# Kernel tuning notes

Hardware: AMD Instinct MI355X
Metric: run time of the kernel (lower is better)

Reference implementation:

```python
import jax, jax.numpy as jnp
import numpy as np
from jax import lax

EPS = 1e-5
ITERS = 10
PPI = 4  # pixels_per_iter


def conv2d(x, w, pad=0, groups=1):
    return lax.conv_general_dilated(
        x, w, (1, 1), [(pad, pad), (pad, pad)],
        dimension_numbers=('NCHW', 'OIHW', 'NCHW'), feature_group_count=groups)


def sep_conv(x, dw, pw):
    # depthwise 3x3 (groups=C) then pointwise 1x1, bias-free
    return conv2d(conv2d(x, dw, pad=1, groups=x.shape[1]), pw)


def maxpool(x, k):
    return lax.reduce_window(x, -jnp.inf, lax.max, (1, 1, k, k), (1, 1, k, k), 'VALID')


def avgpool(x, k):
    return lax.reduce_window(x, 0., lax.add, (1, 1, k, k), (1, 1, k, k), 'VALID') / (k * k)


def grid_sample(img, grid):
    # torch.nn.functional.grid_sample, bilinear, align_corners=True, zeros padding
    # img [B,C,H,W], grid [B,H,W,2] with grid[...,0]=x(width), grid[...,1]=y(height)
    B, C, H, W = img.shape
    x = (grid[..., 0] + 1.) * 0.5 * (W - 1)
    y = (grid[..., 1] + 1.) * 0.5 * (H - 1)
    x0 = jnp.floor(x)
    y0 = jnp.floor(y)
    wx = x - x0
    wy = y - y0

    def corner(xf, yf, w):
        valid = (xf >= 0) & (xf <= W - 1) & (yf >= 0) & (yf <= H - 1)
        xi = jnp.clip(xf, 0, W - 1).astype(jnp.int32)
        yi = jnp.clip(yf, 0, H - 1).astype(jnp.int32)
        v = jax.vmap(lambda im, yy, xx: im[:, yy, xx])(img, yi, xi)  # [B,C,H,W]
        return v * (w * valid)[:, None, :, :]

    return (corner(x0, y0, (1 - wx) * (1 - wy)) + corner(x0 + 1, y0, wx * (1 - wy))
            + corner(x0, y0 + 1, (1 - wx) * wy) + corner(x0 + 1, y0 + 1, wx * wy))


def upmat(n_in, n_out):
    # bilinear interpolation matrix, align_corners=True (UpsamplingBilinear2d)
    pos = jnp.arange(n_out) * ((n_in - 1) / (n_out - 1))
    i0 = jnp.floor(pos).astype(jnp.int32)
    i1 = jnp.minimum(i0 + 1, n_in - 1)
    w = pos - i0
    r = jnp.arange(n_out)
    return jnp.zeros((n_out, n_in), jnp.float32).at[r, i0].add(1 - w).at[r, i1].add(w)


def setup_inputs() -> dict:
    key = jax.random.key(0)
    ks = jax.random.split(key, 12)
    B, Cin, Cout, H, W = 4, 256, 256, 128, 128
    s = 0.05
    d = {}
    d['x'] = jax.random.normal(ks[0], (B, Cin, H, W), jnp.float32)
    d['grads'] = jax.random.normal(ks[1], (B, 2, H, W), jnp.float32)
    d['bn_gamma'] = jnp.ones((Cin,), jnp.float32)
    d['bn_beta'] = jnp.zeros((Cin,), jnp.float32)
    d['bn_mean'] = jnp.zeros((Cin,), jnp.float32)
    d['bn_var'] = jnp.ones((Cin,), jnp.float32)
    d['att1_dw'] = jax.random.normal(ks[2], (Cin, 1, 3, 3), jnp.float32) * s
    d['att1_pw'] = jax.random.normal(ks[3], (Cout, Cin, 1, 1), jnp.float32) * s
    d['att2_dw'] = jax.random.normal(ks[4], (Cin, 1, 3, 3), jnp.float32) * s
    d['att2_pw'] = jax.random.normal(ks[5], (Cout, Cin, 1, 1), jnp.float32) * s
    d['conv1_w'] = jax.random.normal(ks[6], (Cout, Cin, 1, 1), jnp.float32) * s
    d['conv2_w'] = jax.random.normal(ks[7], (Cout, Cin, 1, 1), jnp.float32) * s
    d['add1_w'] = jax.random.normal(ks[8], (Cout, 2 * Cout, 1, 1), jnp.float32) * s
    d['add2_w'] = jax.random.normal(ks[9], (Cout, 2 * Cout, 1, 1), jnp.float32) * s
    d['merge_dw'] = jax.random.normal(ks[10], (2 * Cout, 1, 3, 3), jnp.float32) * s
    d['merge_pw'] = jax.random.normal(ks[11], (Cout, 2 * Cout, 1, 1), jnp.float32) * s
    return d


def reference(x, grads, bn_gamma, bn_beta, bn_mean, bn_var,
              att1_dw, att1_pw, att2_dw, att2_pw, conv1_w, conv2_w,
              add1_w, add2_w, merge_dw, merge_pw):
    # BatchNorm (eval mode, running stats)
    scale = (bn_gamma / jnp.sqrt(bn_var + EPS))[None, :, None, None]
    x = (x - bn_mean[None, :, None, None]) * scale + bn_beta[None, :, None, None]

    a1 = jax.nn.sigmoid(sep_conv(x, att1_dw, att1_pw))
    a2 = jax.nn.sigmoid(sep_conv(x, att2_dw, att2_pw))
    m1 = conv2d(x, conv1_w)
    m2 = conv2d(x, conv2_w)

    a1 = maxpool(a1, PPI)
    a2 = maxpool(a2, PPI)
    m1 = maxpool(m1, PPI)
    m2 = maxpool(m2, PPI)

    B, _, Hd, Wd = m1.shape
    g = avgpool(grads, PPI) / Hd           # [B,2,Hd,Wd]
    g = jnp.transpose(g, (0, 2, 3, 1))      # [B,Hd,Wd,2]

    # identity affine_grid, align_corners=True
    gx = jnp.broadcast_to(jnp.linspace(-1., 1., Wd)[None, None, :], (B, Hd, Wd))
    gy = jnp.broadcast_to(jnp.linspace(-1., 1., Hd)[None, :, None], (B, Hd, Wd))
    base = jnp.stack([gx, gy], axis=-1)
    grid1 = base + g
    grid2 = base - g

    m1 = jax.nn.relu(m1)
    m2 = jax.nn.relu(m2)
    m1_sum, m2_sum = m1, m2
    for _ in range(ITERS):
        m1 = grid_sample(m1, grid1) * a1
        m2 = grid_sample(m2, grid2) * a2
        m1_sum = conv2d(jnp.concatenate([m1_sum, m1], axis=1), add1_w)
        m2_sum = conv2d(jnp.concatenate([m2_sum, m2], axis=1), add2_w)

    out = sep_conv(jnp.concatenate([m1_sum, m2_sum], axis=1) / ITERS, merge_dw, merge_pw)

    Mh = upmat(Hd, Hd * PPI)
    Mw = upmat(Wd, Wd * PPI)
    return jnp.einsum('oh,bchw,pw->bcop', Mh, out, Mw)
```

## Files before the change

kernel.cpp:

```cpp
#include <hip/hip_runtime.h>
#include <cstddef>
#include <cstdint>

#define BN_EPS 1e-5f
typedef unsigned short ushort_t;
typedef __attribute__((ext_vector_type(8))) short bf16x8;
typedef __attribute__((ext_vector_type(4))) float f32x4;

__device__ __forceinline__ ushort_t f2bf(float f) {
  unsigned u = __float_as_uint(f);
  unsigned r = (u + 0x7fffu + ((u >> 16) & 1u)) >> 16;
  return (ushort_t)r;
}
__device__ __forceinline__ float bf2f(ushort_t h) {
  return __uint_as_float(((unsigned)h) << 16);
}
__device__ __forceinline__ void unp8(uint4 u, ushort_t* d) {
  d[0] = u.x & 0xffff; d[1] = u.x >> 16;
  d[2] = u.y & 0xffff; d[3] = u.y >> 16;
  d[4] = u.z & 0xffff; d[5] = u.z >> 16;
  d[6] = u.w & 0xffff; d[7] = u.w >> 16;
}
__device__ __forceinline__ uint4 pk8(const ushort_t* d) {
  uint4 u;
  u.x = (unsigned)d[0] | ((unsigned)d[1] << 16);
  u.y = (unsigned)d[2] | ((unsigned)d[3] << 16);
  u.z = (unsigned)d[4] | ((unsigned)d[5] << 16);
  u.w = (unsigned)d[6] | ((unsigned)d[7] << 16);
  return u;
}

__global__ __launch_bounds__(256) void wsplit_kernel(
    const float* s0, const float* s1, const float* s2, const float* s3,
    const float* s4, const float* s5, const float* s6, ushort_t* d0,
    ushort_t* d1, ushort_t* d2, ushort_t* d3, ushort_t* d4, ushort_t* d5,
    ushort_t* d6) {
  int r = blockIdx.x;
  int tid = threadIdx.x;
  if (r < 1024) {
    int wi = r >> 8, oc = r & 255;
    const float* s = wi == 0 ? s0 : wi == 1 ? s1 : wi == 2 ? s2 : s3;
    ushort_t* d = wi == 0 ? d0 : wi == 1 ? d1 : wi == 2 ? d2 : d3;
    float v = s[oc * 256 + tid];
    ushort_t h = f2bf(v);
// ... 37 lines not shown
    if (rr < 0 || rr > 127) continue;
    const float* rp = base + rr * 128;
    float4 v = reinterpret_cast<const float4*>(rp)[col4];
    v.x = fmaf(v.x, s, sh);
    v.y = fmaf(v.y, s, sh);
    v.z = fmaf(v.z, s, sh);
    v.w = fmaf(v.w, s, sh);
    float lf = col4 ? fmaf(rp[col4 * 4 - 1], s, sh) : 0.f;
    float rg = (col4 < 31) ? fmaf(rp[col4 * 4 + 4], s, sh) : 0.f;
    float k0 = w[(dr + 1) * 3 + 0];
    float k1 = w[(dr + 1) * 3 + 1];
    float k2 = w[(dr + 1) * 3 + 2];
    acc.x = fmaf(k0, lf, fmaf(k1, v.x, fmaf(k2, v.y, acc.x)));
    acc.y = fmaf(k0, v.x, fmaf(k1, v.y, fmaf(k2, v.z, acc.y)));
    acc.z = fmaf(k0, v.y, fmaf(k1, v.z, fmaf(k2, v.w, acc.z)));
    acc.w = fmaf(k0, v.z, fmaf(k1, v.w, fmaf(k2, rg, acc.w)));
  }
  reinterpret_cast<float4*>(out + (size_t)bc * 16384 + row * 128)[col4] = acc;
}

__global__ __launch_bounds__(256) void pw_mfma_kernel(
    const float* __restrict__ src0, const float* __restrict__ src1,
    const ushort_t* __restrict__ W0, const ushort_t* __restrict__ W1,
    ushort_t* __restrict__ o0h, ushort_t* __restrict__ o0l,
    ushort_t* __restrict__ o1h, ushort_t* __restrict__ o1l,
    const float* __restrict__ gamma, const float* __restrict__ beta,
    const float* __restrict__ mean, const float* __restrict__ var, int bnflag,
    int act) {
  __shared__ ushort_t Xh[64 * 40], Xl[64 * 40];
  __shared__ ushort_t Wh[256 * 40], Wl[256 * 40];
  __shared__ float s_lds[256], sh_lds[256];
  const int tid = threadIdx.x;
  const int bx = blockIdx.x;
  const int pr = bx >> 3, pcs = bx & 7;
  const int b = blockIdx.y, z = blockIdx.z;
  const float* src = z ? src1 : src0;
  const ushort_t* Wq = z ? W1 : W0;
  ushort_t* ohi = z ? o1h : o0h;
  ushort_t* olo = z ? o1l : o0l;
  const int R0 = pr * 4, C0 = pcs * 16;
  if (bnflag) {
    float sv = gamma[tid] * rsqrtf(var[tid] + BN_EPS);
    s_lds[tid] = sv;
    sh_lds[tid] = beta[tid] - mean[tid] * sv;
  }
  const int w = tid >> 6, l = tid & 63, lr = l & 15, lh = l >> 4;
  f32x4 acc[4][4];
#pragma unroll
  for (int i = 0; i < 4; i++)
#pragma unroll
    for (int j = 0; j < 4; j++) acc[i][j] = 0.f;

  for (int kc = 0; kc < 8; ++kc) {
    int ic0 = kc * 32;
    __syncthreads();
#pragma unroll
    for (int p = 0; p < 2; ++p) {
      int idx = p * 256 + tid;
      int ic = idx >> 4, rc = idx & 15, r = rc >> 2, c4 = rc & 3;
      const float* gp =
          src + (((size_t)(b * 256 + ic0 + ic) * 128 + R0 + r) * 128 + C0 +
                 c4 * 4);
      float4 v = *(const float4*)gp;
      if (bnflag) {
        float s = s_lds[ic0 + ic], sh = sh_lds[ic0 + ic];
        v.x = fmaf(v.x, s, sh);
        v.y = fmaf(v.y, s, sh);
        v.z = fmaf(v.z, s, sh);
        v.w = fmaf(v.w, s, sh);
      }
      int baserow = c4 * 16 + r * 4;
      const float* vp = &v.x;
#pragma unroll
      for (int q = 0; q < 4; ++q) {
        float f = vp[q];
        ushort_t hv = f2bf(f);
        Xh[(baserow + q) * 40 + ic] = hv;
        Xl[(baserow + q) * 40 + ic] = f2bf(f - bf2f(hv));
      }
    }
#pragma unroll
    for (int p = 0; p < 4; ++p) {
      int i = p * 256 + tid;
      int oc = i >> 2, slot = i & 3;
      *(uint4*)(&Wh[oc * 40 + slot * 8]) =
          *(const uint4*)(Wq + (size_t)oc * 512 + ic0 + slot * 8);
      *(uint4*)(&Wl[oc * 40 + slot * 8]) =
          *(const uint4*)(Wq + (size_t)oc * 512 + 256 + ic0 + slot * 8);
    }
    __syncthreads();
    bf16x8 ah[4], al[4], bh[4], bl[4];
#pragma unroll
    for (int mt = 0; mt < 4; ++mt) {
      ah[mt] = *(const bf16x8*)(&Xh[(mt * 16 + lr) * 40 + lh * 8]);
      al[mt] = *(const bf16x8*)(&Xl[(mt * 16 + lr) * 40 + lh * 8]);
    }
#pragma unroll
    for (int nt = 0; nt < 4; ++nt) {
      bh[nt] = *(const bf16x8*)(&Wh[(w * 64 + nt * 16 + lr) * 40 + lh * 8]);
      bl[nt] = *(const bf16x8*)(&Wl[(w * 64 + nt * 16 + lr) * 40 + lh * 8]);
    }
#pragma unroll
    for (int mt = 0; mt < 4; ++mt)
#pragma unroll
      for (int nt = 0; nt < 4; ++nt)
        acc[mt][nt] = __builtin_amdgcn_mfma_f32_16x16x32_bf16(
            ah[mt], bh[nt], acc[mt][nt], 0, 0, 0);
#pragma unroll
    for (int mt = 0; mt < 4; ++mt)
#pragma unroll
      for (int nt = 0; nt < 4; ++nt)
        acc[mt][nt] = __builtin_amdgcn_mfma_f32_16x16x32_bf16(
            al[mt], bh[nt], acc[mt][nt], 0, 0, 0);
#pragma unroll
    for (int mt = 0; mt < 4; ++mt)
#pragma unroll
      for (int nt = 0; nt < 4; ++nt)
        acc[mt][nt] = __builtin_amdgcn_mfma_f32_16x16x32_bf16(
            ah[mt], bl[nt], acc[mt][nt], 0, 0, 0);
  }
#pragma unroll
  for (int mt = 0; mt < 4; ++mt) {
    int ppx = pr * 32 + pcs * 4 + mt;
#pragma unroll
    for (int nt = 0; nt < 4; ++nt) {
      f32x4 v = acc[mt][nt];
      float m0 = fmaxf(fmaxf(v[0], v[1]), fmaxf(v[2], v[3]));
      m0 = fmaxf(m0, __shfl_xor(m0, 16));
      m0 = fmaxf(m0, __shfl_xor(m0, 32));
      float r = act ? fmaxf(m0, 0.f) : 1.f / (1.f + expf(-m0));
      ushort_t hv = f2bf(r);
      ushort_t lv = f2bf(r - bf2f(hv));
      if (l < 16) {
        size_t o = (size_t)(b * 1024 + ppx) * 256 + w * 64 + nt * 16 + lr;
        ohi[o] = hv;
        olo[o] = lv;
      }
    }
  }
}

__global__ __launch_bounds__(256) void cat_mfma_kernel(
    const ushort_t* Ah0, const ushort_t* Al0, const ushort_t* Bh0,
    const ushort_t* Bl0, const ushort_t* Wq0, ushort_t* oh0, ushort_t* ol0,
    float* of0, const ushort_t* Ah1, const ushort_t* Al1, const ushort_t* Bh1,
    const ushort_t* Bl1, const ushort_t* Wq1, ushort_t* oh1, ushort_t* ol1,
    float* of1, int CA, int sA, int sB, int fout) {
  __shared__ ushort_t Xh[64 * 40], Xl[64 * 40];
  __shared__ ushort_t Wh[128 * 40], Wl[128 * 40];
  __shared__ unsigned obuf[64 * 132];
  const int tid = threadIdx.x;
  const int PX0 = blockIdx.x * 64;
  const int b = blockIdx.y >> 1, OC0 = (blockIdx.y & 1) * 128;
  const int z = blockIdx.z;
  const ushort_t* Ah = z ? Ah1 : Ah0;
  const ushort_t* Al = z ? Al1 : Al0;
  const ushort_t* Bh = z ? Bh1 : Bh0;
  const ushort_t* Bl = z ? Bl1 : Bl0;
  const ushort_t* Wq = z ? Wq1 : Wq0;
  ushort_t* ohi = z ? oh1 : oh0;
  ushort_t* olo = z ? ol1 : ol0;
  float* of = z ? of1 : of0;
  const int w = tid >> 6, l = tid & 63, lr = l & 15, lh = l >> 4;
  f32x4 acc[4][2];
#pragma unroll
  for (int i = 0; i < 4; i++)
#pragma unroll
    for (int j = 0; j < 2; j++) acc[i][j] = 0.f;

  for (int kc = 0; kc < 16; ++kc) {
    int k0 = kc * 32;
    __syncthreads();
    {
      const ushort_t *xh, *xl;
      int cc0, st;
      if (k0 < CA) {
        xh = Ah; xl = Al; cc0 = k0; st = sA;
      } else {
        xh = Bh; xl = Bl; cc0 = k0 - CA; st = sB;
      }
      int px = tid >> 2, slot = tid & 3;
      size_t xo = (size_t)(b * 1024 + PX0 + px) * st + cc0 + slot * 8;
      *(uint4*)(&Xh[px * 40 + slot * 8]) = *(const uint4*)(xh + xo);
      *(uint4*)(&Xl[px * 40 + slot * 8]) = *(const uint4*)(xl + xo);
    }
#pragma unroll
    for (int p = 0; p < 2; ++p) {
      int i = p * 256 + tid;
      int oc = i >> 2, slot = i & 3;
      *(uint4*)(&Wh[oc * 40 + slot * 8]) =
          *(const uint4*)(Wq + (size_t)(OC0 + oc) * 1024 + k0 + slot * 8);
      *(uint4*)(&Wl[oc * 40 + slot * 8]) = *(const uint4*)(
          Wq + (size_t)(OC0 + oc) * 1024 + 512 + k0 + slot * 8);
    }
    __syncthreads();
    bf16x8 ah[4], al[4], bh[2], bl[2];
#pragma unroll
    for (int mt = 0; mt < 4; ++mt) {
      ah[mt] = *(const bf16x8*)(&Xh[(mt * 16 + lr) * 40 + lh * 8]);
      al[mt] = *(const bf16x8*)(&Xl[(mt * 16 + lr) * 40 + lh * 8]);
    }
#pragma unroll
    for (int nt = 0; nt < 2; ++nt) {
      bh[nt] = *(const bf16x8*)(&Wh[(w * 32 + nt * 16 + lr) * 40 + lh * 8]);
      bl[nt] = *(const bf16x8*)(&Wl[(w * 32 + nt * 16 + lr) * 40 + lh * 8]);
    }
#pragma unroll
    for (int mt = 0; mt < 4; ++mt)
#pragma unroll
      for (int nt = 0; nt < 2; ++nt)
        acc[mt][nt] = __builtin_amdgcn_mfma_f32_16x16x32_bf16(
            ah[mt], bh[nt], acc[mt][nt], 0, 0, 0);
#pragma unroll
    for (int mt = 0; mt < 4; ++mt)
#pragma unroll
      for (int nt = 0; nt < 2; ++nt)
        acc[mt][nt] = __builtin_amdgcn_mfma_f32_16x16x32_bf16(
            al[mt], bh[nt], acc[mt][nt], 0, 0, 0);
#pragma unroll
    for (int mt = 0; mt < 4; ++mt)
#pragma unroll
      for (int nt = 0; nt < 2; ++nt)
        acc[mt][nt] = __builtin_amdgcn_mfma_f32_16x16x32_bf16(
            ah[mt], bl[nt], acc[mt][nt], 0, 0, 0);
  }
  if (fout) {
#pragma unroll
    for (int mt = 0; mt < 4; ++mt)
#pragma unroll
      for (int nt = 0; nt < 2; ++nt) {
        int oc = OC0 + w * 32 + nt * 16 + lr;
        int px0 = PX0 + mt * 16 + lh * 4;
        float4 vv = make_float4(acc[mt][nt][0], acc[mt][nt][1], acc[mt][nt][2],
                                acc[mt][nt][3]);
        *(float4*)(of + ((size_t)(b * 256 + oc) * 1024 + px0)) = vv;
      }
  } else {
    __syncthreads();
#pragma unroll
    for (int mt = 0; mt < 4; ++mt)
#pragma unroll
      for (int nt = 0; nt < 2; ++nt)
#pragma unroll
        for (int j = 0; j < 4; ++j) {
          float f = acc[mt][nt][j];
          ushort_t hv = f2bf(f);
          ushort_t lv = f2bf(f - bf2f(hv));
          obuf[(mt * 16 + lh * 4 + j) * 132 + w * 32 + nt * 16 + lr] =
              (unsigned)hv | ((unsigned)lv << 16);
        }
    __syncthreads();
    int px = tid >> 2;
#pragma unroll
    for (int g = 0; g < 4; ++g) {
      int og = (tid & 3) * 32 + g * 8;
      ushort_t h8[8], l8[8];
#pragma unroll
      for (int q = 0; q < 8; ++q) {
        unsigned u = obuf[px * 132 + og + q];
        h8[q] = u & 0xffff;
        l8[q] = u >> 16;
      }
      size_t o = (size_t)(b * 1024 + PX0 + px) * 256 + OC0 + og;
      *(uint4*)(ohi + o) = pk8(h8);
      *(uint4*)(olo + o) = pk8(l8);
    }
  }
}

__global__ void grads_pool_kernel(const float* __restrict__ grads,
                                  int4* __restrict__ pxi1,
                                  float4* __restrict__ w1,
                                  int4* __restrict__ pxi2,
                                  float4* __restrict__ w2) {
  unsigned flat = blockIdx.x * 256u + threadIdx.x;
  unsigned pw = flat & 31u, ph = (flat >> 5) & 31u, b = flat >> 10;
  const float* gx = grads + (size_t)(b * 2 + 0) * 16384;
  const float* gy = grads + (size_t)(b * 2 + 1) * 16384;
  float sx_ = 0.f, sy_ = 0.f;
#pragma unroll
  for (int r = 0; r < 4; r++) {
    const float* rx = gx + (ph * 4 + r) * 128 + pw * 4;
    const float* ry = gy + (ph * 4 + r) * 128 + pw * 4;
#pragma unroll
    for (int q = 0; q < 4; q++) {
      sx_ += rx[q];
      sy_ += ry[q];
    }
  }
// ... 14 lines not shown
    bool vx1 = (x0f + 1.f >= 0.f) && (x0f + 1.f <= 31.f);
    bool vy0 = (y0f >= 0.f) && (y0f <= 31.f);
    bool vy1 = (y0f + 1.f >= 0.f) && (y0f + 1.f <= 31.f);
    int x0c = min(max(x0, 0), 31), x1c = min(max(x0 + 1, 0), 31);
    int y0c = min(max(y0, 0), 31), y1c = min(max(y0 + 1, 0), 31);
    int4 pi = make_int4(y0c * 32 + x0c, y0c * 32 + x1c, y1c * 32 + x0c,
                        y1c * 32 + x1c);
    float4 ww =
        make_float4((1.f - wx) * (1.f - wy) * ((vx0 && vy0) ? 1.f : 0.f),
                    wx * (1.f - wy) * ((vx1 && vy0) ? 1.f : 0.f),
                    (1.f - wx) * wy * ((vx0 && vy1) ? 1.f : 0.f),
                    wx * wy * ((vx1 && vy1) ? 1.f : 0.f));
    if (s == 0) {
      pxi1[sidx] = pi;
      w1[sidx] = ww;
    } else {
      pxi2[sidx] = pi;
      w2[sidx] = ww;
    }
  }
}

__global__ __launch_bounds__(256) void gs_mul_kernel(
    const ushort_t* c0h, const ushort_t* c0l, const ushort_t* a0h,
    const ushort_t* a0l, const int4* pxi0, const float4* wg0, ushort_t* o0h,
    ushort_t* o0l, const ushort_t* c1h, const ushort_t* c1l,
    const ushort_t* a1h, const ushort_t* a1l, const int4* pxi1,
    const float4* wg1, ushort_t* o1h, ushort_t* o1l) {
  unsigned flat = blockIdx.x * 256u + threadIdx.x;
  unsigned cg = flat & 31u;
  unsigned px = (flat >> 5) & 1023u;
  unsigned b = (flat >> 15) & 3u;
  unsigned br = flat >> 17;
  const ushort_t* ch = br ? c1h : c0h;
  const ushort_t* cl = br ? c1l : c0l;
  const ushort_t* ah = br ? a1h : a0h;
  const ushort_t* al = br ? a1l : a0l;
  const int4* pxi = br ? pxi1 : pxi0;
  const float4* wg = br ? wg1 : wg0;
  ushort_t* ohp = br ? o1h : o0h;
  ushort_t* olp = br ? o1l : o0l;
  int4 pi = pxi[b * 1024 + px];
  float4 wv = wg[b * 1024 + px];
  size_t rb = (size_t)b * 1024;
  int co = cg * 8;
  float v[8];
#pragma unroll
  for (int j = 0; j < 8; ++j) v[j] = 0.f;
  const int rows[4] = {pi.x, pi.y, pi.z, pi.w};
  const float wks[4] = {wv.x, wv.y, wv.z, wv.w};
#pragma unroll
  for (int k = 0; k < 4; ++k) {
    size_t o = (rb + rows[k]) * 256 + co;
    uint4 hu = *(const uint4*)(ch + o);
    uint4 lu = *(const uint4*)(cl + o);
    ushort_t h8[8], l8[8];
    unp8(hu, h8);
    unp8(lu, l8);
    float wk = wks[k];
#pragma unroll
    for (int j = 0; j < 8; ++j)
      v[j] = fmaf(wk, bf2f(h8[j]) + bf2f(l8[j]), v[j]);
  }
  size_t oo = (rb + px) * 256 + co;
  uint4 ahu = *(const uint4*)(ah + oo);
  uint4 alu = *(const uint4*)(al + oo);
  ushort_t ah8[8], al8[8];
  unp8(ahu, ah8);
  unp8(alu, al8);
  ushort_t rh[8], rl[8];
#pragma unroll
  for (int j = 0; j < 8; ++j) {
    float r = v[j] * (bf2f(ah8[j]) + bf2f(al8[j]));
    rh[j] = f2bf(r);
    rl[j] = f2bf(r - bf2f(rh[j]));
  }
  *(uint4*)(ohp + oo) = pk8(rh);
  *(uint4*)(olp + oo) = pk8(rl);
}

__global__ __launch_bounds__(256) void merge_dw_kernel(
    const ushort_t* s1h, const ushort_t* s1l, const ushort_t* s2h,
    const ushort_t* s2l, const float* __restrict__ wall, ushort_t* dh,
    ushort_t* dl) {
  __shared__ float wlds[576];
  int bx = blockIdx.x;
  int pr = bx >> 3, cset = bx & 7;
  int b = blockIdx.y;
  int pc = threadIdx.x & 31, cg = threadIdx.x >> 5;
  for (int i = threadIdx.x; i < 576; i += 256) wlds[i] = wall[cset * 576 + i];
  __syncthreads();
  const ushort_t* sh_ = (cset < 4) ? s1h : s2h;
  const ushort_t* sl_ = (cset < 4) ? s1l : s2l;
  int csrc = (cset & 3) * 64 + cg * 8;
  float acc[8];
#pragma unroll
  for (int j = 0; j < 8; ++j) acc[j] = 0.f;
#pragma unroll
  for (int dr = -1; dr <= 1; ++dr) {
    int r2 = pr + dr;
    if (r2 < 0 || r2 > 31) continue;
#pragma unroll
    for (int dc = -1; dc <= 1; ++dc) {
      int c2 = pc + dc;
      if (c2 < 0 || c2 > 31) continue;
      size_t o = ((size_t)(b * 1024) + r2 * 32 + c2) * 256 + csrc;
      uint4 hu = *(const uint4*)(sh_ + o);
      uint4 lu = *(const uint4*)(sl_ + o);
      ushort_t h8[8], l8[8];
      unp8(hu, h8);
      unp8(lu, l8);
      int wi = (dr + 1) * 3 + (dc + 1);
#pragma unroll
      for (int j = 0; j < 8; ++j)
        acc[j] = fmaf(wlds[(cg * 8 + j) * 9 + wi], bf2f(h8[j]) + bf2f(l8[j]),
                      acc[j]);
    }
  }
  size_t oo = ((size_t)(b * 1024) + pr * 32 + pc) * 512 + cset * 64 + cg * 8;
  ushort_t h8[8], l8[8];
#pragma unroll
  for (int j = 0; j < 8; ++j) {
    float f = acc[j] * 0.1f;
    h8[j] = f2bf(f);
    l8[j] = f2bf(f - bf2f(h8[j]));
  }
  *(uint4*)(dh + oo) = pk8(h8);
  *(uint4*)(dl + oo) = pk8(l8);
}

__global__ __launch_bounds__(256) void upsample_kernel(
    const float* __restrict__ mid, float* __restrict__ out) {
  unsigned flat = blockIdx.x * 256u + threadIdx.x;
  unsigned ow4 = flat & 31u;
  unsigned oh = (flat >> 5) & 127u;
  unsigned bc = flat >> 12;
  const float* pl = mid + (size_t)bc * 1024;
  float rh = oh * (31.f / 127.f);
  float ihf = floorf(rh);
  float wh = rh - ihf;
  int i0 = (int)ihf;
  int i1 = min(i0 + 1, 31);
  const float* r0 = pl + i0 * 32;
  const float* r1 = pl + i1 * 32;
  float4 res;
  float* rp = &res.x;
#pragma unroll
  for (int j = 0; j < 4; j++) {
    unsigned ow = ow4 * 4 + j;
    float rw = ow * (31.f / 127.f);
    float jwf = floorf(rw);
// ... 23 lines not shown
  const float* att1_dw = (const float*)d_in[6];
  const float* att1_pw = (const float*)d_in[7];
  const float* att2_dw = (const float*)d_in[8];
  const float* att2_pw = (const float*)d_in[9];
  const float* conv1_w = (const float*)d_in[10];
  const float* conv2_w = (const float*)d_in[11];
  const float* add1_w = (const float*)d_in[12];
  const float* add2_w = (const float*)d_in[13];
  const float* merge_dww = (const float*)d_in[14];
  const float* merge_pww = (const float*)d_in[15];
  float* out = (float*)d_out;

  const size_t MB = 1u << 20;
  uint8_t* base = (uint8_t*)d_ws;
  float* t1 = (float*)base;
  uint8_t* P = base + 64 * MB;
  ushort_t* wAtt1 = (ushort_t*)P; P += 262144;
  ushort_t* wAtt2 = (ushort_t*)P; P += 262144;
  ushort_t* wC1 = (ushort_t*)P; P += 262144;
  ushort_t* wC2 = (ushort_t*)P; P += 262144;
  ushort_t* wAdd1 = (ushort_t*)P; P += 524288;
  ushort_t* wAdd2 = (ushort_t*)P; P += 524288;
  ushort_t* wMrg = (ushort_t*)P; P += 524288;
  ushort_t* a1h = (ushort_t*)P; P += 2 * MB;
  ushort_t* a1l = (ushort_t*)P; P += 2 * MB;
  ushort_t* a2h = (ushort_t*)P; P += 2 * MB;
  ushort_t* a2l = (ushort_t*)P; P += 2 * MB;
  ushort_t* m1Ph = (ushort_t*)P; P += 2 * MB;
  ushort_t* m1Pl = (ushort_t*)P; P += 2 * MB;
  ushort_t* m2Ph = (ushort_t*)P; P += 2 * MB;
  ushort_t* m2Pl = (ushort_t*)P; P += 2 * MB;
  int4* pxi1 = (int4*)P; P += 65536;
  float4* w1g = (float4*)P; P += 65536;
  int4* pxi2 = (int4*)P; P += 65536;
  float4* w2g = (float4*)P; P += 65536;
  uint8_t* Q = base;
  ushort_t* m1Qh = (ushort_t*)Q; Q += 2 * MB;
  ushort_t* m1Ql = (ushort_t*)Q; Q += 2 * MB;
  ushort_t* m2Qh = (ushort_t*)Q; Q += 2 * MB;
  ushort_t* m2Ql = (ushort_t*)Q; Q += 2 * MB;
  ushort_t* s1ah = (ushort_t*)Q; Q += 2 * MB;
  ushort_t* s1al = (ushort_t*)Q; Q += 2 * MB;
  ushort_t* s1bh = (ushort_t*)Q; Q += 2 * MB;
  ushort_t* s1bl = (ushort_t*)Q; Q += 2 * MB;
  ushort_t* s2ah = (ushort_t*)Q; Q += 2 * MB;
  ushort_t* s2al = (ushort_t*)Q; Q += 2 * MB;
  ushort_t* s2bh = (ushort_t*)Q; Q += 2 * MB;
  ushort_t* s2bl = (ushort_t*)Q; Q += 2 * MB;
  ushort_t* dwmh = (ushort_t*)Q; Q += 4 * MB;
  ushort_t* dwml = (ushort_t*)Q; Q += 4 * MB;
  float* mid = (float*)Q; Q += 4 * MB;

  wsplit_kernel<<<1792, 256, 0, stream>>>(att1_pw, att2_pw, conv1_w, conv2_w,
                                          add1_w, add2_w, merge_pww, wAtt1,
                                          wAtt2, wC1, wC2, wAdd1, wAdd2, wMrg);
  pw_mfma_kernel<<<dim3(256, 4, 2), 256, 0, stream>>>(
      x, x, wC1, wC2, m1Ph, m1Pl, m2Ph, m2Pl, bn_gamma, bn_beta, bn_mean,
      bn_var, 1, 1);
  dw_bn_kernel<<<16384, 256, 0, stream>>>(x, att1_dw, bn_gamma, bn_beta,
                                          bn_mean, bn_var, t1);
  pw_mfma_kernel<<<dim3(256, 4, 1), 256, 0, stream>>>(
      t1, t1, wAtt1, wAtt1, a1h, a1l, a1h, a1l, bn_gamma, bn_beta, bn_mean,
      bn_var, 0, 0);
  dw_bn_kernel<<<16384, 256, 0, stream>>>(x, att2_dw, bn_gamma, bn_beta,
                                          bn_mean, bn_var, t1);
  pw_mfma_kernel<<<dim3(256, 4, 1), 256, 0, stream>>>(
      t1, t1, wAtt2, wAtt2, a2h, a2l, a2h, a2l, bn_gamma, bn_beta, bn_mean,
      bn_var, 0, 0);
  grads_pool_kernel<<<16, 256, 0, stream>>>(grads, pxi1, w1g, pxi2, w2g);

  const ushort_t *c1h = m1Ph, *c1l = m1Pl, *c2h = m2Ph, *c2l = m2Pl;
  const ushort_t *ss1h = m1Ph, *ss1l = m1Pl, *ss2h = m2Ph, *ss2l = m2Pl;
  for (int it = 0; it < 10; ++it) {
    ushort_t* n1h = (it & 1) ? m1Ph : m1Qh;
    ushort_t* n1l = (it & 1) ? m1Pl : m1Ql;
    ushort_t* n2h = (it & 1) ? m2Ph : m2Qh;
    ushort_t* n2l = (it & 1) ? m2Pl : m2Ql;
    gs_mul_kernel<<<1024, 256, 0, stream>>>(c1h, c1l, a1h, a1l, pxi1, w1g, n1h,
                                            n1l, c2h, c2l, a2h, a2l, pxi2, w2g,
                                            n2h, n2l);
    ushort_t* so1h = (it & 1) ? s1bh : s1ah;
    ushort_t* so1l = (it & 1) ? s1bl : s1al;
    ushort_t* so2h = (it & 1) ? s2bh : s2ah;
    ushort_t* so2l = (it & 1) ? s2bl : s2al;
    cat_mfma_kernel<<<dim3(16, 8, 2), 256, 0, stream>>>(
        ss1h, ss1l, n1h, n1l, wAdd1, so1h, so1l, nullptr, ss2h, ss2l, n2h, n2l,
        wAdd2, so2h, so2l, nullptr, 256, 256, 256, 0);
    c1h = n1h; c1l = n1l; c2h = n2h; c2l = n2l;
    ss1h = so1h; ss1l = so1l; ss2h = so2h; ss2l = so2l;
  }
  merge_dw_kernel<<<dim3(256, 4), 256, 0, stream>>>(ss1h, ss1l, ss2h, ss2l,
                                                    merge_dww, dwmh, dwml);
  cat_mfma_kernel<<<dim3(16, 8, 1), 256, 0, stream>>>(
      dwmh, dwml, dwmh, dwml, wMrg, nullptr, nullptr, mid, dwmh, dwml, dwmh,
      dwml, wMrg, nullptr, nullptr, mid, 512, 512, 512, 1);
  upsample_kernel<<<16384, 256, 0, stream>>>(mid, out);
}
```

Measured before the change: 704.3 us.

## Interleave bf16 hi/lo pairs, prefetch GEMM tiles, shrink cat kernel tiles

Split-bf16 activations now use one interleaved 32-bit hi/lo word per value instead of two separate planes. Every producer and consumer (gs_mul, merge_dw, pointwise and cat GEMMs) switches to single vector loads and stores of the packed pairs. The pw and cat MFMA kernels register-prefetch the next K chunk while computing the current one. The cat kernel is replaced by a 128-thread, 32x64-tile version with direct global stores instead of the LDS-staged output transpose. This aims to cut memory transactions and hide load latency, but the direct scattered 4-byte output stores may be less coalesced.

After: 663.9 us. 5.7% less time.

```diff
diff --git a/kernel.cpp b/kernel.cpp
--- a/kernel.cpp
+++ b/kernel.cpp
@@ -15,11 +15,12 @@
 __device__ __forceinline__ float bf2f(ushort_t h) {
   return __uint_as_float(((unsigned)h) << 16);
 }
-__device__ __forceinline__ void unp8(uint4 u, ushort_t* d) {
-  d[0] = u.x & 0xffff; d[1] = u.x >> 16;
-  d[2] = u.y & 0xffff; d[3] = u.y >> 16;
-  d[4] = u.z & 0xffff; d[5] = u.z >> 16;
-  d[6] = u.w & 0xffff; d[7] = u.w >> 16;
+__device__ __forceinline__ float upk(unsigned u) {
+  return bf2f((ushort_t)(u & 0xffff)) + bf2f((ushort_t)(u >> 16));
+}
+__device__ __forceinline__ unsigned pkpair(float f) {
+  ushort_t h = f2bf(f);
+  return (unsigned)h | ((unsigned)f2bf(f - bf2f(h)) << 16);
 }
 __device__ __forceinline__ uint4 pk8(const ushort_t* d) {
   uint4 u;
@@ -103,8 +104,7 @@
 __global__ __launch_bounds__(256) void pw_mfma_kernel(
     const float* __restrict__ src0, const float* __restrict__ src1,
     const ushort_t* __restrict__ W0, const ushort_t* __restrict__ W1,
-    ushort_t* __restrict__ o0h, ushort_t* __restrict__ o0l,
-    ushort_t* __restrict__ o1h, ushort_t* __restrict__ o1l,
+    unsigned* __restrict__ o0, unsigned* __restrict__ o1,
     const float* __restrict__ gamma, const float* __restrict__ beta,
     const float* __restrict__ mean, const float* __restrict__ var, int bnflag,
     int act) {
@@ -117,14 +117,17 @@
   const int b = blockIdx.y, z = blockIdx.z;
   const float* src = z ? src1 : src0;
   const ushort_t* Wq = z ? W1 : W0;
-  ushort_t* ohi = z ? o1h : o0h;
-  ushort_t* olo = z ? o1l : o0l;
+  unsigned* op = z ? o1 : o0;
   const int R0 = pr * 4, C0 = pcs * 16;
   if (bnflag) {
     float sv = gamma[tid] * rsqrtf(var[tid] + BN_EPS);
     s_lds[tid] = sv;
     sh_lds[tid] = beta[tid] - mean[tid] * sv;
-  }
+  } else {
+    s_lds[tid] = 1.f;
+    sh_lds[tid] = 0.f;
+  }
+  __syncthreads();
   const int w = tid >> 6, l = tid & 63, lr = l & 15, lh = l >> 4;
   f32x4 acc[4][4];
 #pragma unroll
@@ -132,24 +135,34 @@
 #pragma unroll
     for (int j = 0; j < 4; j++) acc[i][j] = 0.f;
 
-  for (int kc = 0; kc < 8; ++kc) {
+  float4 xf0, xf1;
+  auto LDXP = [&](int kc) {
     int ic0 = kc * 32;
-    __syncthreads();
+    {
+      int idx = tid;
+      int ic = idx >> 4, rc = idx & 15, r = rc >> 2, c4 = rc & 3;
+      xf0 = *(const float4*)(src + (((size_t)(b * 256 + ic0 + ic) * 128 + R0 +
+                                     r) * 128 + C0 + c4 * 4));
+    }
+    {
+      int idx = 256 + tid;
+      int ic = idx >> 4, rc = idx & 15, r = rc >> 2, c4 = rc & 3;
+      xf1 = *(const float4*)(src + (((size_t)(b * 256 + ic0 + ic) * 128 + R0 +
+                                     r) * 128 + C0 + c4 * 4));
+    }
+  };
+  auto WRXP = [&](int kc) {
+    int ic0 = kc * 32;
 #pragma unroll
     for (int p = 0; p < 2; ++p) {
       int idx = p * 256 + tid;
       int ic = idx >> 4, rc = idx & 15, r = rc >> 2, c4 = rc & 3;
-      const float* gp =
-          src + (((size_t)(b * 256 + ic0 + ic) * 128 + R0 + r) * 128 + C0 +
-                 c4 * 4);
-      float4 v = *(const float4*)gp;
-      if (bnflag) {
-        float s = s_lds[ic0 + ic], sh = sh_lds[ic0 + ic];
-        v.x = fmaf(v.x, s, sh);
-        v.y = fmaf(v.y, s, sh);
-        v.z = fmaf(v.z, s, sh);
-        v.w = fmaf(v.w, s, sh);
-      }
+      float4 v = p ? xf1 : xf0;
+      float s = s_lds[ic0 + ic], sh = sh_lds[ic0 + ic];
+      v.x = fmaf(v.x, s, sh);
+      v.y = fmaf(v.y, s, sh);
+      v.z = fmaf(v.z, s, sh);
+      v.w = fmaf(v.w, s, sh);
       int baserow = c4 * 16 + r * 4;
       const float* vp = &v.x;
 #pragma unroll
@@ -160,6 +173,9 @@
         Xl[(baserow + q) * 40 + ic] = f2bf(f - bf2f(hv));
       }
     }
+  };
+  auto WSTG = [&](int kc) {
+    int ic0 = kc * 32;
 #pragma unroll
     for (int p = 0; p < 4; ++p) {
       int i = p * 256 + tid;
@@ -169,7 +185,13 @@
       *(uint4*)(&Wl[oc * 40 + slot * 8]) =
           *(const uint4*)(Wq + (size_t)oc * 512 + 256 + ic0 + slot * 8);
     }
-    __syncthreads();
+  };
+  LDXP(0);
+  WRXP(0);
+  WSTG(0);
+  __syncthreads();
+  for (int kc = 0; kc < 8; ++kc) {
+    if (kc < 7) LDXP(kc + 1);
     bf16x8 ah[4], al[4], bh[4], bl[4];
 #pragma unroll
     for (int mt = 0; mt < 4; ++mt) {
@@ -199,6 +221,12 @@
       for (int nt = 0; nt < 4; ++nt)
         acc[mt][nt] = __builtin_amdgcn_mfma_f32_16x16x32_bf16(
             ah[mt], bl[nt], acc[mt][nt], 0, 0, 0);
+    if (kc < 7) {
+      __syncthreads();
+      WRXP(kc + 1);
+      WSTG(kc + 1);
+      __syncthreads();
+    }
   }
 #pragma unroll
   for (int mt = 0; mt < 4; ++mt) {
@@ -210,74 +238,83 @@
       m0 = fmaxf(m0, __shfl_xor(m0, 16));
       m0 = fmaxf(m0, __shfl_xor(m0, 32));
       float r = act ? fmaxf(m0, 0.f) : 1.f / (1.f + expf(-m0));
-      ushort_t hv = f2bf(r);
-      ushort_t lv = f2bf(r - bf2f(hv));
-      if (l < 16) {
-        size_t o = (size_t)(b * 1024 + ppx) * 256 + w * 64 + nt * 16 + lr;
-        ohi[o] = hv;
-        olo[o] = lv;
-      }
-    }
-  }
-}
-
-__global__ __launch_bounds__(256) void cat_mfma_kernel(
-    const ushort_t* Ah0, const ushort_t* Al0, const ushort_t* Bh0,
-    const ushort_t* Bl0, const ushort_t* Wq0, ushort_t* oh0, ushort_t* ol0,
-    float* of0, const ushort_t* Ah1, const ushort_t* Al1, const ushort_t* Bh1,
-    const ushort_t* Bl1, const ushort_t* Wq1, ushort_t* oh1, ushort_t* ol1,
-    float* of1, int CA, int sA, int sB, int fout) {
-  __shared__ ushort_t Xh[64 * 40], Xl[64 * 40];
-  __shared__ ushort_t Wh[128 * 40], Wl[128 * 40];
-  __shared__ unsigned obuf[64 * 132];
+      if (l < 16)
+        op[(size_t)(b * 1024 + ppx) * 256 + w * 64 + nt * 16 + lr] = pkpair(r);
+    }
+  }
+}
+
+__global__ __launch_bounds__(128) void catp_kernel(
+    const unsigned* A0, const unsigned* B0, const ushort_t* W0, unsigned* op0,
+    float* of0, const unsigned* A1, const unsigned* B1, const ushort_t* W1,
+    unsigned* op1, float* of1, int CA, int sA, int sB, int fout) {
+  __shared__ ushort_t Xh[32 * 40], Xl[32 * 40];
+  __shared__ ushort_t Wh[64 * 40], Wl[64 * 40];
   const int tid = threadIdx.x;
-  const int PX0 = blockIdx.x * 64;
-  const int b = blockIdx.y >> 1, OC0 = (blockIdx.y & 1) * 128;
+  const int strip = blockIdx.x;
+  const int b = strip >> 5;
+  const int PX0 = (strip & 31) * 32;
+  const int OC0 = blockIdx.y * 64;
   const int z = blockIdx.z;
-  const ushort_t* Ah = z ? Ah1 : Ah0;
-  const ushort_t* Al = z ? Al1 : Al0;
-  const ushort_t* Bh = z ? Bh1 : Bh0;
-  const ushort_t* Bl = z ? Bl1 : Bl0;
-  const ushort_t* Wq = z ? Wq1 : Wq0;
-  ushort_t* ohi = z ? oh1 : oh0;
-  ushort_t* olo = z ? ol1 : ol0;
+  const unsigned* A = z ? A1 : A0;
+  const unsigned* B = z ? B1 : B0;
+  const ushort_t* Wq = z ? W1 : W0;
+  unsigned* op = z ? op1 : op0;
   float* of = z ? of1 : of0;
   const int w = tid >> 6, l = tid & 63, lr = l & 15, lh = l >> 4;
-  f32x4 acc[4][2];
-#pragma unroll
-  for (int i = 0; i < 4; i++)
+  const int spx = tid >> 2, sslot = tid & 3;
+  const int soc = tid >> 1, shalf = tid & 1;
+  uint4 xr0, xr1, w0h, w1h, w0l, w1l;
+  f32x4 acc[2][2];
+#pragma unroll
+  for (int i = 0; i < 2; i++)
 #pragma unroll
     for (int j = 0; j < 2; j++) acc[i][j] = 0.f;
 
+  auto LDX = [&](int kc) {
+    int k0 = kc * 32;
+    const unsigned* src;
+    int cc0, st;
+    if (k0 < CA) {
+      src = A; cc0 = k0; st = sA;
+    } else {
+      src = B; cc0 = k0 - CA; st = sB;
+    }
+    const unsigned* p =
+        src + ((size_t)(b * 1024 + PX0 + spx) * st + cc0 + sslot * 8);
+    xr0 = *(const uint4*)p;
+    xr1 = *(const uint4*)(p + 4);
+    const ushort_t* wp = Wq + (size_t)(OC0 + soc) * 1024 + k0 + shalf * 16;
+    w0h = *(const uint4*)wp;
+    w1h = *(const uint4*)(wp + 8);
+    w0l = *(const uint4*)(wp + 512);
+    w1l = *(const uint4*)(wp + 520);
+  };
+  auto WRX = [&]() {
+    ushort_t h8[8], l8[8];
+    h8[0] = xr0.x & 0xffff; l8[0] = xr0.x >> 16;
+    h8[1] = xr0.y & 0xffff; l8[1] = xr0.y >> 16;
+    h8[2] = xr0.z & 0xffff; l8[2] = xr0.z >> 16;
+    h8[3] = xr0.w & 0xffff; l8[3] = xr0.w >> 16;
+    h8[4] = xr1.x & 0xffff; l8[4] = xr1.x >> 16;
+    h8[5] = xr1.y & 0xffff; l8[5] = xr1.y >> 16;
+    h8[6] = xr1.z & 0xffff; l8[6] = xr1.z >> 16;
+    h8[7] = xr1.w & 0xffff; l8[7] = xr1.w >> 16;
+    *(uint4*)(&Xh[spx * 40 + sslot * 8]) = pk8(h8);
+    *(uint4*)(&Xl[spx * 40 + sslot * 8]) = pk8(l8);
+    *(uint4*)(&Wh[soc * 40 + shalf * 16]) = w0h;
+    *(uint4*)(&Wh[soc * 40 + shalf * 16 + 8]) = w1h;
+    *(uint4*)(&Wl[soc * 40 + shalf * 16]) = w0l;
+    *(uint4*)(&Wl[soc * 40 + shalf * 16 + 8]) = w1l;
+  };
+  LDX(0);
+  WRX();
+  __syncthreads();
   for (int kc = 0; kc < 16; ++kc) {
-    int k0 = kc * 32;
-    __syncthreads();
-    {
-      const ushort_t *xh, *xl;
-      int cc0, st;
-      if (k0 < CA) {
-        xh = Ah; xl = Al; cc0 = k0; st = sA;
-      } else {
-        xh = Bh; xl = Bl; cc0 = k0 - CA; st = sB;
-      }
-      int px = tid >> 2, slot = tid & 3;
-      size_t xo = (size_t)(b * 1024 + PX0 + px) * st + cc0 + slot * 8;
-      *(uint4*)(&Xh[px * 40 + slot * 8]) = *(const uint4*)(xh + xo);
-      *(uint4*)(&Xl[px * 40 + slot * 8]) = *(const uint4*)(xl + xo);
-    }
-#pragma unroll
-    for (int p = 0; p < 2; ++p) {
-      int i = p * 256 + tid;
-      int oc = i >> 2, slot = i & 3;
-      *(uint4*)(&Wh[oc * 40 + slot * 8]) =
-          *(const uint4*)(Wq + (size_t)(OC0 + oc) * 1024 + k0 + slot * 8);
-      *(uint4*)(&Wl[oc * 40 + slot * 8]) = *(const uint4*)(
-          Wq + (size_t)(OC0 + oc) * 1024 + 512 + k0 + slot * 8);
-    }
-    __syncthreads();
-    bf16x8 ah[4], al[4], bh[2], bl[2];
-#pragma unroll
-    for (int mt = 0; mt < 4; ++mt) {
+    if (kc < 15) LDX(kc + 1);
+    bf16x8 ah[2], al[2], bh[2], bl[2];
+#pragma unroll
+    for (int mt = 0; mt < 2; ++mt) {
       ah[mt] = *(const bf16x8*)(&Xh[(mt * 16 + lr) * 40 + lh * 8]);
       al[mt] = *(const bf16x8*)(&Xl[(mt * 16 + lr) * 40 + lh * 8]);
     }
@@ -287,27 +324,25 @@
       bl[nt] = *(const bf16x8*)(&Wl[(w * 32 + nt * 16 + lr) * 40 + lh * 8]);
     }
 #pragma unroll
-    for (int mt = 0; mt < 4; ++mt)
-#pragma unroll
-      for (int nt = 0; nt < 2; ++nt)
+    for (int mt = 0; mt < 2; ++mt)
+#pragma unroll
+      for (int nt = 0; nt < 2; ++nt) {
         acc[mt][nt] = __builtin_amdgcn_mfma_f32_16x16x32_bf16(
             ah[mt], bh[nt], acc[mt][nt], 0, 0, 0);
-#pragma unroll
-    for (int mt = 0; mt < 4; ++mt)
-#pragma unroll
-      for (int nt = 0; nt < 2; ++nt)
         acc[mt][nt] = __builtin_amdgcn_mfma_f32_16x16x32_bf16(
             al[mt], bh[nt], acc[mt][nt], 0, 0, 0);
-#pragma unroll
-    for (int mt = 0; mt < 4; ++mt)
-#pragma unroll
-      for (int nt = 0; nt < 2; ++nt)
         acc[mt][nt] = __builtin_amdgcn_mfma_f32_16x16x32_bf16(
             ah[mt], bl[nt], acc[mt][nt], 0, 0, 0);
+      }
+    if (kc < 15) {
+      __syncthreads();
+      WRX();
+      __syncthreads();
+    }
   }
   if (fout) {
 #pragma unroll
-    for (int mt = 0; mt < 4; ++mt)
+    for (int mt = 0; mt < 2; ++mt)
 #pragma unroll
       for (int nt = 0; nt < 2; ++nt) {
         int oc = OC0 + w * 32 + nt * 16 + lr;
@@ -317,35 +352,17 @@
         *(float4*)(of + ((size_t)(b * 256 + oc) * 1024 + px0)) = vv;
       }
   } else {
-    __syncthreads();
-#pragma unroll
-    for (int mt = 0; mt < 4; ++mt)
-#pragma unroll
-      for (int nt = 0; nt < 2; ++nt)
+#pragma unroll
+    for (int mt = 0; mt < 2; ++mt)
+#pragma unroll
+      for (int nt = 0; nt < 2; ++nt) {
+        int oc = OC0 + w * 32 + nt * 16 + lr;
 #pragma unroll
         for (int j = 0; j < 4; ++j) {
-          float f = acc[mt][nt][j];
-          ushort_t hv = f2bf(f);
-          ushort_t lv = f2bf(f - bf2f(hv));
-          obuf[(mt * 16 + lh * 4 + j) * 132 + w * 32 + nt * 16 + lr] =
-              (unsigned)hv | ((unsigned)lv << 16);
+          int px = PX0 + mt * 16 + lh * 4 + j;
+          op[(size_t)(b * 1024 + px) * 256 + oc] = pkpair(acc[mt][nt][j]);
         }
-    __syncthreads();
-    int px = tid >> 2;
-#pragma unroll
-    for (int g = 0; g < 4; ++g) {
-      int og = (tid & 3) * 32 + g * 8;
-      ushort_t h8[8], l8[8];
-#pragma unroll
-      for (int q = 0; q < 8; ++q) {
-        unsigned u = obuf[px * 132 + og + q];
-        h8[q] = u & 0xffff;
-        l8[q] = u >> 16;
       }
-      size_t o = (size_t)(b * 1024 + PX0 + px) * 256 + OC0 + og;
-      *(uint4*)(ohi + o) = pk8(h8);
-      *(uint4*)(olo + o) = pk8(l8);
-    }
   }
 }
 
@@ -406,24 +423,19 @@
 }
 
 __global__ __launch_bounds__(256) void gs_mul_kernel(
-    const ushort_t* c0h, const ushort_t* c0l, const ushort_t* a0h,
-    const ushort_t* a0l, const int4* pxi0, const float4* wg0, ushort_t* o0h,
-    ushort_t* o0l, const ushort_t* c1h, const ushort_t* c1l,
-    const ushort_t* a1h, const ushort_t* a1l, const int4* pxi1,
-    const float4* wg1, ushort_t* o1h, ushort_t* o1l) {
+    const unsigned* c0, const unsigned* a0, const int4* pxi0,
+    const float4* wg0, unsigned* o0, const unsigned* c1, const unsigned* a1,
+    const int4* pxi1, const float4* wg1, unsigned* o1) {
   unsigned flat = blockIdx.x * 256u + threadIdx.x;
   unsigned cg = flat & 31u;
   unsigned px = (flat >> 5) & 1023u;
   unsigned b = (flat >> 15) & 3u;
   unsigned br = flat >> 17;
-  const ushort_t* ch = br ? c1h : c0h;
-  const ushort_t* cl = br ? c1l : c0l;
-  const ushort_t* ah = br ? a1h : a0h;
-  const ushort_t* al = br ? a1l : a0l;
+  const unsigned* c = br ? c1 : c0;
+  const unsigned* a = br ? a1 : a0;
   const int4* pxi = br ? pxi1 : pxi0;
   const float4* wg = br ? wg1 : wg0;
-  ushort_t* ohp = br ? o1h : o0h;
-  ushort_t* olp = br ? o1l : o0l;
+  unsigned* o = br ? o1 : o0;
   int4 pi = pxi[b * 1024 + px];
   float4 wv = wg[b * 1024 + px];
   size_t rb = (size_t)b * 1024;
@@ -435,38 +447,38 @@
   const float wks[4] = {wv.x, wv.y, wv.z, wv.w};
 #pragma unroll
   for (int k = 0; k < 4; ++k) {
-    size_t o = (rb + rows[k]) * 256 + co;
-    uint4 hu = *(const uint4*)(ch + o);
-    uint4 lu = *(const uint4*)(cl + o);
-    ushort_t h8[8], l8[8];
-    unp8(hu, h8);
-    unp8(lu, l8);
+    const unsigned* p = c + (rb + rows[k]) * 256 + co;
+    uint4 u0 = *(const uint4*)p;
+    uint4 u1 = *(const uint4*)(p + 4);
     float wk = wks[k];
-#pragma unroll
-    for (int j = 0; j < 8; ++j)
-      v[j] = fmaf(wk, bf2f(h8[j]) + bf2f(l8[j]), v[j]);
+    v[0] = fmaf(wk, upk(u0.x), v[0]);
+    v[1] = fmaf(wk, upk(u0.y), v[1]);
+    v[2] = fmaf(wk, upk(u0.z), v[2]);
+    v[3] = fmaf(wk, upk(u0.w), v[3]);
+    v[4] = fmaf(wk, upk(u1.x), v[4]);
+    v[5] = fmaf(wk, upk(u1.y), v[5]);
+    v[6] = fmaf(wk, upk(u1.z), v[6]);
+    v[7] = fmaf(wk, upk(u1.w), v[7]);
   }
   size_t oo = (rb + px) * 256 + co;
-  uint4 ahu = *(const uint4*)(ah + oo);
-  uint4 alu = *(const uint4*)(al + oo);
-  ushort_t ah8[8], al8[8];
-  unp8(ahu, ah8);
-  unp8(alu, al8);
-  ushort_t rh[8], rl[8];
-#pragma unroll
-  for (int j = 0; j < 8; ++j) {
-    float r = v[j] * (bf2f(ah8[j]) + bf2f(al8[j]));
-    rh[j] = f2bf(r);
-    rl[j] = f2bf(r - bf2f(rh[j]));
-  }
-  *(uint4*)(ohp + oo) = pk8(rh);
-  *(uint4*)(olp + oo) = pk8(rl);
+  uint4 au0 = *(const uint4*)(a + oo);
+  uint4 au1 = *(const uint4*)(a + oo + 4);
+  uint4 r0, r1;
+  r0.x = pkpair(v[0] * upk(au0.x));
+  r0.y = pkpair(v[1] * upk(au0.y));
+  r0.z = pkpair(v[2] * upk(au0.z));
+  r0.w = pkpair(v[3] * upk(au0.w));
+  r1.x = pkpair(v[4] * upk(au1.x));
+  r1.y = pkpair(v[5] * upk(au1.y));
+  r1.z = pkpair(v[6] * upk(au1.z));
+  r1.w = pkpair(v[7] * upk(au1.w));
+  *(uint4*)(o + oo) = r0;
+  *(uint4*)(o + oo + 4) = r1;
 }
 
 __global__ __launch_bounds__(256) void merge_dw_kernel(
-    const ushort_t* s1h, const ushort_t* s1l, const ushort_t* s2h,
-    const ushort_t* s2l, const float* __restrict__ wall, ushort_t* dh,
-    ushort_t* dl) {
+    const unsigned* s1, const unsigned* s2, const float* __restrict__ wall,
+    unsigned* d) {
   __shared__ float wlds[576];
   int bx = blockIdx.x;
   int pr = bx >> 3, cset = bx & 7;
@@ -474,8 +486,7 @@
   int pc = threadIdx.x & 31, cg = threadIdx.x >> 5;
   for (int i = threadIdx.x; i < 576; i += 256) wlds[i] = wall[cset * 576 + i];
   __syncthreads();
-  const ushort_t* sh_ = (cset < 4) ? s1h : s2h;
-  const ushort_t* sl_ = (cset < 4) ? s1l : s2l;
+  const unsigned* sp = (cset < 4) ? s1 : s2;
   int csrc = (cset & 3) * 64 + cg * 8;
   float acc[8];
 #pragma unroll
@@ -488,29 +499,32 @@
     for (int dc = -1; dc <= 1; ++dc) {
       int c2 = pc + dc;
       if (c2 < 0 || c2 > 31) continue;
-      size_t o = ((size_t)(b * 1024) + r2 * 32 + c2) * 256 + csrc;
-      uint4 hu = *(const uint4*)(sh_ + o);
-      uint4 lu = *(const uint4*)(sl_ + o);
-      ushort_t h8[8], l8[8];
-      unp8(hu, h8);
-      unp8(lu, l8);
+      const unsigned* p = sp + ((size_t)(b * 1024) + r2 * 32 + c2) * 256 + csrc;
+      uint4 u0 = *(const uint4*)p;
+      uint4 u1 = *(const uint4*)(p + 4);
       int wi = (dr + 1) * 3 + (dc + 1);
-#pragma unroll
-      for (int j = 0; j < 8; ++j)
-        acc[j] = fmaf(wlds[(cg * 8 + j) * 9 + wi], bf2f(h8[j]) + bf2f(l8[j]),
-                      acc[j]);
+      acc[0] = fmaf(wlds[(cg * 8 + 0) * 9 + wi], upk(u0.x), acc[0]);
+      acc[1] = fmaf(wlds[(cg * 8 + 1) * 9 + wi], upk(u0.y), acc[1]);
+      acc[2] = fmaf(wlds[(cg * 8 + 2) * 9 + wi], upk(u0.z), acc[2]);
+      acc[3] = fmaf(wlds[(cg * 8 + 3) * 9 + wi], upk(u0.w), acc[3]);
+      acc[4] = fmaf(wlds[(cg * 8 + 4) * 9 + wi], upk(u1.x), acc[4]);
+      acc[5] = fmaf(wlds[(cg * 8 + 5) * 9 + wi], upk(u1.y), acc[5]);
+      acc[6] = fmaf(wlds[(cg * 8 + 6) * 9 + wi], upk(u1.z), acc[6]);
+      acc[7] = fmaf(wlds[(cg * 8 + 7) * 9 + wi], upk(u1.w), acc[7]);
     }
   }
   size_t oo = ((size_t)(b * 1024) + pr * 32 + pc) * 512 + cset * 64 + cg * 8;
-  ushort_t h8[8], l8[8];
-#pragma unroll
-  for (int j = 0; j < 8; ++j) {
-    float f = acc[j] * 0.1f;
-    h8[j] = f2bf(f);
-    l8[j] = f2bf(f - bf2f(h8[j]));
-  }
-  *(uint4*)(dh + oo) = pk8(h8);
-  *(uint4*)(dl + oo) = pk8(l8);
+  uint4 r0, r1;
+  r0.x = pkpair(acc[0] * 0.1f);
+  r0.y = pkpair(acc[1] * 0.1f);
+  r0.z = pkpair(acc[2] * 0.1f);
+  r0.w = pkpair(acc[3] * 0.1f);
+  r1.x = pkpair(acc[4] * 0.1f);
+  r1.y = pkpair(acc[5] * 0.1f);
+  r1.z = pkpair(acc[6] * 0.1f);
+  r1.w = pkpair(acc[7] * 0.1f);
+  *(uint4*)(d + oo) = r0;
+  *(uint4*)(d + oo + 4) = r1;
 }
 
 __global__ __launch_bounds__(256) void upsample_kernel(
@@ -580,77 +594,60 @@
   ushort_t* wAdd1 = (ushort_t*)P; P += 524288;
   ushort_t* wAdd2 = (ushort_t*)P; P += 524288;
   ushort_t* wMrg = (ushort_t*)P; P += 524288;
-  ushort_t* a1h = (ushort_t*)P; P += 2 * MB;
-  ushort_t* a1l = (ushort_t*)P; P += 2 * MB;
-  ushort_t* a2h = (ushort_t*)P; P += 2 * MB;
-  ushort_t* a2l = (ushort_t*)P; P += 2 * MB;
-  ushort_t* m1Ph = (ushort_t*)P; P += 2 * MB;
-  ushort_t* m1Pl = (ushort_t*)P; P += 2 * MB;
-  ushort_t* m2Ph = (ushort_t*)P; P += 2 * MB;
-  ushort_t* m2Pl = (ushort_t*)P; P += 2 * MB;
+  unsigned* a1p = (unsigned*)P; P += 4 * MB;
+  unsigned* a2p = (unsigned*)P; P += 4 * MB;
+  unsigned* m1P = (unsigned*)P; P += 4 * MB;
+  unsigned* m2P = (unsigned*)P; P += 4 * MB;
   int4* pxi1 = (int4*)P; P += 65536;
   float4* w1g = (float4*)P; P += 65536;
   int4* pxi2 = (int4*)P; P += 65536;
   float4* w2g = (float4*)P; P += 65536;
   uint8_t* Q = base;
-  ushort_t* m1Qh = (ushort_t*)Q; Q += 2 * MB;
-  ushort_t* m1Ql = (ushort_t*)Q; Q += 2 * MB;
-  ushort_t* m2Qh = (ushort_t*)Q; Q += 2 * MB;
-  ushort_t* m2Ql = (ushort_t*)Q; Q += 2 * MB;
-  ushort_t* s1ah = (ushort_t*)Q; Q += 2 * MB;
-  ushort_t* s1al = (ushort_t*)Q; Q += 2 * MB;
-  ushort_t* s1bh = (ushort_t*)Q; Q += 2 * MB;
-  ushort_t* s1bl = (ushort_t*)Q; Q += 2 * MB;
-  ushort_t* s2ah = (ushort_t*)Q; Q += 2 * MB;
-  ushort_t* s2al = (ushort_t*)Q; Q += 2 * MB;
-  ushort_t* s2bh = (ushort_t*)Q; Q += 2 * MB;
-  ushort_t* s2bl = (ushort_t*)Q; Q += 2 * MB;
-  ushort_t* dwmh = (ushort_t*)Q; Q += 4 * MB;
-  ushort_t* dwml = (ushort_t*)Q; Q += 4 * MB;
+  unsigned* m1Q = (unsigned*)Q; Q += 4 * MB;
+  unsigned* m2Q = (unsigned*)Q; Q += 4 * MB;
+  unsigned* s1a = (unsigned*)Q; Q += 4 * MB;
+  unsigned* s1b = (unsigned*)Q; Q += 4 * MB;
+  unsigned* s2a = (unsigned*)Q; Q += 4 * MB;
+  unsigned* s2b = (unsigned*)Q; Q += 4 * MB;
+  unsigned* dwm = (unsigned*)Q; Q += 8 * MB;
   float* mid = (float*)Q; Q += 4 * MB;
 
   wsplit_kernel<<<1792, 256, 0, stream>>>(att1_pw, att2_pw, conv1_w, conv2_w,
                                           add1_w, add2_w, merge_pww, wAtt1,
                                           wAtt2, wC1, wC2, wAdd1, wAdd2, wMrg);
   pw_mfma_kernel<<<dim3(256, 4, 2), 256, 0, stream>>>(
-      x, x, wC1, wC2, m1Ph, m1Pl, m2Ph, m2Pl, bn_gamma, bn_beta, bn_mean,
-      bn_var, 1, 1);
+      x, x, wC1, wC2, m1P, m2P, bn_gamma, bn_beta, bn_mean, bn_var, 1, 1);
   dw_bn_kernel<<<16384, 256, 0, stream>>>(x, att1_dw, bn_gamma, bn_beta,
                                           bn_mean, bn_var, t1);
   pw_mfma_kernel<<<dim3(256, 4, 1), 256, 0, stream>>>(
-      t1, t1, wAtt1, wAtt1, a1h, a1l, a1h, a1l, bn_gamma, bn_beta, bn_mean,
-      bn_var, 0, 0);
+      t1, t1, wAtt1, wAtt1, a1p, a1p, bn_gamma, bn_beta, bn_mean, bn_var, 0,
+      0);
   dw_bn_kernel<<<16384, 256, 0, stream>>>(x, att2_dw, bn_gamma, bn_beta,
                                           bn_mean, bn_var, t1);
   pw_mfma_kernel<<<dim3(256, 4, 1), 256, 0, stream>>>(
-      t1, t1, wAtt2, wAtt2, a2h, a2l, a2h, a2l, bn_gamma, bn_beta, bn_mean,
-      bn_var, 0, 0);
+      t1, t1, wAtt2, wAtt2, a2p, a2p, bn_gamma, bn_beta, bn_mean, bn_var, 0,
+      0);
   grads_pool_kernel<<<16, 256, 0, stream>>>(grads, pxi1, w1g, pxi2, w2g);
 
-  const ushort_t *c1h = m1Ph, *c1l = m1Pl, *c2h = m2Ph, *c2l = m2Pl;
-  const ushort_t *ss1h = m1Ph, *ss1l = m1Pl, *ss2h = m2Ph, *ss2l = m2Pl;
+  const unsigned *c1 = m1P, *c2 = m2P, *ss1 = m1P, *ss2 = m2P;
   for (int it = 0; it < 10; ++it) {
-    ushort_t* n1h = (it & 1) ? m1Ph : m1Qh;
-    ushort_t* n1l = (it & 1) ? m1Pl : m1Ql;
-    ushort_t* n2h = (it & 1) ? m2Ph : m2Qh;
-    ushort_t* n2l = (it & 1) ? m2Pl : m2Ql;
-    gs_mul_kernel<<<1024, 256, 0, stream>>>(c1h, c1l, a1h, a1l, pxi1, w1g, n1h,
-                                            n1l, c2h, c2l, a2h, a2l, pxi2, w2g,
-                                            n2h, n2l);
-    ushort_t* so1h = (it & 1) ? s1bh : s1ah;
-    ushort_t* so1l = (it & 1) ? s1bl : s1al;
-    ushort_t* so2h = (it & 1) ? s2bh : s2ah;
-    ushort_t* so2l = (it & 1) ? s2bl : s2al;
-    cat_mfma_kernel<<<dim3(16, 8, 2), 256, 0, stream>>>(
-        ss1h, ss1l, n1h, n1l, wAdd1, so1h, so1l, nullptr, ss2h, ss2l, n2h, n2l,
-        wAdd2, so2h, so2l, nullptr, 256, 256, 256, 0);
-    c1h = n1h; c1l = n1l; c2h = n2h; c2l = n2l;
-    ss1h = so1h; ss1l = so1l; ss2h = so2h; ss2l = so2l;
-  }
-  merge_dw_kernel<<<dim3(256, 4), 256, 0, stream>>>(ss1h, ss1l, ss2h, ss2l,
-                                                    merge_dww, dwmh, dwml);
-  cat_mfma_kernel<<<dim3(16, 8, 1), 256, 0, stream>>>(
-      dwmh, dwml, dwmh, dwml, wMrg, nullptr, nullptr, mid, dwmh, dwml, dwmh,
-      dwml, wMrg, nullptr, nullptr, mid, 512, 512, 512, 1);
+    unsigned* n1 = (it & 1) ? m1P : m1Q;
+    unsigned* n2 = (it & 1) ? m2P : m2Q;
+    gs_mul_kernel<<<1024, 256, 0, stream>>>(c1, a1p, pxi1, w1g, n1, c2, a2p,
+                                            pxi2, w2g, n2);
+    unsigned* so1 = (it & 1) ? s1b : s1a;
+    unsigned* so2 = (it & 1) ? s2b : s2a;
+    catp_kernel<<<dim3(128, 4, 2), 128, 0, stream>>>(
+        ss1, n1, wAdd1, so1, nullptr, ss2, n2, wAdd2, so2, nullptr, 256, 256,
+        256, 0);
+    c1 = n1;
+    c2 = n2;
+    ss1 = so1;
+    ss2 = so2;
+  }
+  merge_dw_kernel<<<dim3(256, 4), 256, 0, stream>>>(ss1, ss2, merge_dww, dwm);
+  catp_kernel<<<dim3(128, 4, 1), 128, 0, stream>>>(
+      dwm, dwm, wMrg, nullptr, mid, dwm, dwm, wMrg, nullptr, mid, 512, 512,
+      512, 1);
   upsample_kernel<<<16384, 256, 0, stream>>>(mid, out);
 }
```
